# Optimization experiments

Hardware: AMD Instinct MI355X
Metric: run time of the kernel (lower is better)

The kernel has to match this reference:

```python
import jax, jax.numpy as jnp
import numpy as np

NUM_STEPS = 8
ADD_IDENTITY = True
EPS = 1e-12
STANDARDIZE = True


def setup_inputs() -> dict:
    key = jax.random.key(0)
    N = 4096
    E = 65536  # avg degree 16
    edge_index = jax.random.randint(key, (2, E), 0, N, dtype=jnp.int64 if jax.config.jax_enable_x64 else jnp.int32)
    edge_weight = jnp.ones((E,), dtype=jnp.float32)
    return {"edge_index": edge_index, "edge_weight": edge_weight, "num_nodes": N}


def reference(edge_index, edge_weight, num_nodes):
    # A[i,j] = sum of edge_weight over edges (row=i, col=j); scipy sums duplicates,
    # and segment_sum does the same.
    row, col = edge_index[0], edge_index[1]
    # deg_j = column sums of A (A.sum(axis=0))
    deg = jax.ops.segment_sum(edge_weight, col, num_segments=num_nodes)
    deg = jnp.maximum(deg, EPS)
    # M = A @ D^{-1}:  M[row, col] = w / deg[col]
    w = edge_weight / deg[col]  # [E]

    # Carry dense propagator P = M^t, extract diagonals for t = 1..NUM_STEPS.
    P0 = jnp.eye(num_nodes, dtype=jnp.float32)  # [N, N]

    def step(P, _):
        # P_new[i, :] = sum_{edges (i=row, j=col)} w_e * P[j, :]
        P = jax.ops.segment_sum(w[:, None] * P[col], row, num_segments=num_nodes)
        return P, jnp.diagonal(P)

    _, diags = jax.lax.scan(step, P0, None, length=NUM_STEPS)  # [T, N]

    X = diags.T  # [N, T]
    if ADD_IDENTITY:
        X = jnp.concatenate([jnp.ones((num_nodes, 1), dtype=jnp.float32), X], axis=1)
    if STANDARDIZE:
        mean = X.mean(axis=0, keepdims=True)
        std = jnp.maximum(X.std(axis=0, keepdims=True), 1e-6)  # ddof=0 == unbiased=False
        X = (X - mean) / std
    return X
```

## Files before the change

kernel.cpp:

```cpp
#include <hip/hip_runtime.h>

#define NN 4096
#define TSTEPS 8
#define EPSW 1e-12f
#define SLABW 512
#define NSLAB 8
#define LSLAB 9
#define SLAB_ELEMS ((size_t)NN * SLABW)

typedef unsigned int uint32;
typedef uint32 uint4v __attribute__((ext_vector_type(4)));

__device__ __forceinline__ uint32 bf16rn(float f) {
  uint32 b = __float_as_uint(f);
  return (b + 0x7FFFu + ((b >> 16) & 1u)) >> 16;
}
__device__ __forceinline__ float bf2f(ushort u) {
  return __uint_as_float(((uint32)u) << 16);
}
__device__ __forceinline__ float rdlanef(float v, int k) {
  return __uint_as_float(__builtin_amdgcn_readlane(__float_as_uint(v), k));
}
__device__ __forceinline__ int sphys(int c) {
  int blk = c >> 3;
  return ((blk ^ ((blk >> 3) & 7)) << 3) | (c & 7);
}

__global__ __launch_bounds__(256) void deg_counts_kernel(
    const int* __restrict__ rows, const int* __restrict__ cols,
    const float* __restrict__ ew, float* __restrict__ deg,
    int* __restrict__ counts, int E) {
  int e = blockIdx.x * 256 + threadIdx.x;
  if (e >= E) return;
  atomicAdd(deg + cols[e], ew[e]);
  atomicAdd(counts + rows[e], 1);
}

__global__ __launch_bounds__(1024) void scan_kernel(const int* __restrict__ counts,
                                                    int* __restrict__ row_ptr) {
  __shared__ int sm[1024];
  int tid = threadIdx.x;
  int b = tid * 4;
  int c0 = counts[b], c1 = counts[b + 1], c2 = counts[b + 2], c3 = counts[b + 3];
  sm[tid] = c0 + c1 + c2 + c3;
  __syncthreads();
  for (int off = 1; off < 1024; off <<= 1) {
    int v = (tid >= off) ? sm[tid - off] : 0;
    __syncthreads();
    sm[tid] += v;
    __syncthreads();
  }
  int excl = (tid == 0) ? 0 : sm[tid - 1];
  row_ptr[b]     = excl;
  row_ptr[b + 1] = excl + c0;
  row_ptr[b + 2] = excl + c0 + c1;
  row_ptr[b + 3] = excl + c0 + c1 + c2;
  if (tid == 1023) row_ptr[NN] = sm[1023];
}

__global__ __launch_bounds__(256) void csr_scatter_kernel(
    const int* __restrict__ rows, const int* __restrict__ cols,
    const float* __restrict__ ew, const float* __restrict__ deg,
    const int* __restrict__ row_ptr, int* __restrict__ fill,
    int* __restrict__ col_s, float* __restrict__ w_s,
    float* __restrict__ diags, int E) {
  int e = blockIdx.x * 256 + threadIdx.x;
  if (e >= E) return;
  int r = rows[e], c = cols[e];
  float w = ew[e] / fmaxf(deg[c], EPSW);
  int pos = row_ptr[r] + atomicAdd(fill + r, 1);
  col_s[pos] = c;
  w_s[pos] = w;
  if (r == c) atomicAdd(diags + r, w);
}

__global__ __launch_bounds__(64) void m2_csr_kernel(
    const int* __restrict__ row_ptr, const int* __restrict__ col_s,
    const float* __restrict__ w_s, ushort* __restrict__ dst,
    float* __restrict__ diags) {
  int i = blockIdx.x;
  int tid = threadIdx.x;
  __shared__ float acc[NN];
  float4 z4 = make_float4(0.f, 0.f, 0.f, 0.f);
#pragma unroll
  for (int k = 0; k < 16; ++k) *(float4*)(acc + k * 256 + tid * 4) = z4;
  int e0 = row_ptr[i], e1 = row_ptr[i + 1];
  __syncthreads();
  for (int base = e0; base < e1; base += 64) {
    int cnt = min(64, e1 - base);
    int myc = 0;
    float myw = 0.f;
    if (tid < cnt) { myc = col_s[base + tid]; myw = w_s[base + tid]; }
    for (int e = 0; e < cnt; ++e) {
      int j = __builtin_amdgcn_readlane(myc, e);
      float we = rdlanef(myw, e);
      int f0 = row_ptr[j], f1 = row_ptr[j + 1];
      for (int f = f0 + tid; f < f1; f += 64)
        atomicAdd(acc + sphys(col_s[f]), we * w_s[f]);
    }
  }
  __syncthreads();
  if (tid == 0) diags[NN + i] = acc[sphys(i)];
#pragma unroll
  for (int p = 0; p < 8; ++p) {
    int c = p * SLABW + tid * 8;
    int ph = sphys(c);
    float4 lo = *(const float4*)(acc + ph);
    float4 hi = *(const float4*)(acc + ph + 4);
    uint4v o;
    o.x = bf16rn(lo.x) | (bf16rn(lo.y) << 16);
    o.y = bf16rn(lo.z) | (bf16rn(lo.w) << 16);
    o.z = bf16rn(hi.x) | (bf16rn(hi.y) << 16);
    o.w = bf16rn(hi.z) | (bf16rn(hi.w) << 16);
    __builtin_nontemporal_store(
        o, (uint4v*)(dst + (size_t)p * SLAB_ELEMS + (size_t)i * SLABW + tid * 8));
  }
}

#define FMA8(u, w)                                            \
  do {                                                        \
    _Pragma("unroll") for (int q = 0; q < 4; ++q) {           \
      acc[2 * q]     += (w) * __uint_as_float((u)[q] << 16);  \
      acc[2 * q + 1] += (w) * __uint_as_float((u)[q] & 0xFFFF0000u); \
    }                                                         \
  } while (0)

__global__ __launch_bounds__(256) void spmm_kernel(
    const ushort* __restrict__ src, ushort* __restrict__ dst,
    const int* __restrict__ row_ptr, const int* __restrict__ col_s,
    const float* __restrict__ w_s, float* __restrict__ diags, int tIdx) {
  int b = blockIdx.x;
  int slab = b & (NSLAB - 1);
  int wv = threadIdx.x >> 6;
  int lane = threadIdx.x & 63;
  int i = ((b >> 3) << 2) | wv;
  int e0 = row_ptr[i], e1 = row_ptr[i + 1];
  __shared__ int sc_all[4][64];
  __shared__ float sw_all[4][64];
  int* sc = sc_all[wv];
  float* sw = sw_all[wv];
  float acc[8];
#pragma unroll
  for (int q = 0; q < 8; ++q) acc[q] = 0.f;
  const ushort* sbase = src + (size_t)slab * SLAB_ELEMS + lane * 8;

  for (int base = e0; base < e1; base += 64) {
    int cnt = min(64, e1 - base);
    if (lane < cnt) {
      sc[lane] = col_s[base + lane];
      sw[lane] = w_s[base + lane];
    }
    int k = 0;
    for (; k + 8 <= cnt; k += 8) {
      uint4v u0 = *(const uint4v*)(sbase + ((size_t)sc[k]     << LSLAB));
      uint4v u1 = *(const uint4v*)(sbase + ((size_t)sc[k + 1] << LSLAB));
      uint4v u2 = *(const uint4v*)(sbase + ((size_t)sc[k + 2] << LSLAB));
      uint4v u3 = *(const uint4v*)(sbase + ((size_t)sc[k + 3] << LSLAB));
      uint4v u4 = *(const uint4v*)(sbase + ((size_t)sc[k + 4] << LSLAB));
      uint4v u5 = *(const uint4v*)(sbase + ((size_t)sc[k + 5] << LSLAB));
      uint4v u6 = *(const uint4v*)(sbase + ((size_t)sc[k + 6] << LSLAB));
      uint4v u7 = *(const uint4v*)(sbase + ((size_t)sc[k + 7] << LSLAB));
      float w0 = sw[k], w1 = sw[k + 1], w2 = sw[k + 2], w3 = sw[k + 3];
      float w4 = sw[k + 4], w5 = sw[k + 5], w6 = sw[k + 6], w7 = sw[k + 7];
      FMA8(u0, w0); FMA8(u1, w1); FMA8(u2, w2); FMA8(u3, w3);
      FMA8(u4, w4); FMA8(u5, w5); FMA8(u6, w6); FMA8(u7, w7);
    }
    for (; k + 4 <= cnt; k += 4) {
      uint4v u0 = *(const uint4v*)(sbase + ((size_t)sc[k]     << LSLAB));
      uint4v u1 = *(const uint4v*)(sbase + ((size_t)sc[k + 1] << LSLAB));
      uint4v u2 = *(const uint4v*)(sbase + ((size_t)sc[k + 2] << LSLAB));
      uint4v u3 = *(const uint4v*)(sbase + ((size_t)sc[k + 3] << LSLAB));
      float w0 = sw[k], w1 = sw[k + 1], w2 = sw[k + 2], w3 = sw[k + 3];
      FMA8(u0, w0); FMA8(u1, w1); FMA8(u2, w2); FMA8(u3, w3);
    }
    for (; k < cnt; ++k) {
      uint4v u = *(const uint4v*)(sbase + ((size_t)sc[k] << LSLAB));
      float w = sw[k];
      FMA8(u, w);
    }
  }

  uint4v o;
#pragma unroll
  for (int q = 0; q < 4; ++q)
    o[q] = bf16rn(acc[2 * q]) | (bf16rn(acc[2 * q + 1]) << 16);
  __builtin_nontemporal_store(
      o, (uint4v*)(dst + (size_t)slab * SLAB_ELEMS + (size_t)i * SLABW + lane * 8));

  if ((i >> LSLAB) == slab) {
    int lc = i & (SLABW - 1);
    if ((lc >> 3) == lane) {
      int m = lc & 7;
      float v = acc[0];
      v = (m == 1) ? acc[1] : v;
      v = (m == 2) ? acc[2] : v;
      v = (m == 3) ? acc[3] : v;
      v = (m == 4) ? acc[4] : v;
      v = (m == 5) ? acc[5] : v;
      v = (m == 6) ? acc[6] : v;
      v = (m == 7) ? acc[7] : v;
      diags[tIdx * NN + i] = v;
    }
  }
}

__device__ __forceinline__ size_t slab_addr(int row, int col) {
  return ((size_t)(col >> LSLAB)) * SLAB_ELEMS + (size_t)row * SLABW + (col & (SLABW - 1));
}
__device__ __forceinline__ float elem8(uint4v lo, uint4v hi, int c) {
  uint32 u = (c < 8) ? lo[(c & 7) >> 1] : hi[(c & 7) >> 1];
  return __uint_as_float((c & 1) ? (u & 0xFFFF0000u) : (u << 16));
}

__global__ __launch_bounds__(256) void trace_kernel(
    const ushort* __restrict__ M2, const ushort* __restrict__ M3,
    const ushort* __restrict__ M4, float* __restrict__ diags) {
  int bid = blockIdx.x;
  int bi = bid >> 3, jc = bid & 7;
  int tid = threadIdx.x;
  __shared__ ushort b3[64 * 64], b4[64 * 64];
  __shared__ float red[4][4][64];
  int lr = tid >> 2, lc0 = (tid & 3) * 16;
  int r = tid & 63, jq = tid >> 6;
  float s5 = 0.f, s6 = 0.f, s7 = 0.f, s8 = 0.f;

  for (int it = 0; it < 8; ++it) {
    int bj = jc * 8 + it;
    {
      int gj = bj * 64 + lr;
      int gc = bi * 64 + lc0;
      size_t base = slab_addr(gj, gc);
      uint4v v3a = *(const uint4v*)(M3 + base);
      uint4v v3b = *(const uint4v*)(M3 + base + 8);
      uint4v v4a = *(const uint4v*)(M4 + base);
      uint4v v4b = *(const uint4v*)(M4 + base + 8);
      int cb0 = (lc0 >> 3) ^ (lr & 7);
      int cb1 = ((lc0 >> 3) + 1) ^ (lr & 7);
      *(uint4v*)(b3 + lr * 64 + cb0 * 8) = v3a;
      *(uint4v*)(b3 + lr * 64 + cb1 * 8) = v3b;
      *(uint4v*)(b4 + lr * 64 + cb0 * 8) = v4a;
      *(uint4v*)(b4 + lr * 64 + cb1 * 8) = v4b;
    }
    __syncthreads();
    int gi = bi * 64 + r;
    int gc0 = bj * 64 + jq * 16;
    size_t abase = slab_addr(gi, gc0);
    uint4v a2a = *(const uint4v*)(M2 + abase);
    uint4v a2b = *(const uint4v*)(M2 + abase + 8);
    uint4v a3a = *(const uint4v*)(M3 + abase);
    uint4v a3b = *(const uint4v*)(M3 + abase + 8);
    uint4v a4a = *(const uint4v*)(M4 + abase);
    uint4v a4b = *(const uint4v*)(M4 + abase + 8);
#pragma unroll
    for (int c = 0; c < 16; ++c) {
      int jj = jq * 16 + c;
      int idx = jj * 64 + ((((r >> 3) ^ (jj & 7)) << 3) | (r & 7));
      float bv3 = bf2f(b3[idx]);
      float bv4 = bf2f(b4[idx]);
      float av2 = elem8(a2a, a2b, c);
      float av3 = elem8(a3a, a3b, c);
      float av4 = elem8(a4a, a4b, c);
      s5 += av2 * bv3;
      s6 += av3 * bv3;
      s7 += av3 * bv4;
      s8 += av4 * bv4;
    }
    __syncthreads();
  }
  red[0][jq][r] = s5;
  red[1][jq][r] = s6;
  red[2][jq][r] = s7;
  red[3][jq][r] = s8;
  __syncthreads();
  if (tid < 64) {
    int gi = bi * 64 + tid;
#pragma unroll
    for (int v = 0; v < 4; ++v) {
      float s = red[v][0][tid] + red[v][1][tid] + red[v][2][tid] + red[v][3][tid];
      atomicAdd(diags + (4 + v) * NN + gi, s);
    }
  }
}

__global__ __launch_bounds__(256) void finalize_kernel(const float* __restrict__ diags,
                                                       float* __restrict__ out) {
  int k = blockIdx.x;
  int tid = threadIdx.x;
  float vals[16];
  float sum = 0.f, sq = 0.f;
#pragma unroll
  for (int j = 0; j < 16; ++j) {
    int i = j * 256 + tid;
    float v = (k == 0) ? 1.0f : diags[(k - 1) * NN + i];
    vals[j] = v;
    sum += v;
    sq += v * v;
  }
#pragma unroll
  for (int off = 32; off; off >>= 1) {
    sum += __shfl_down(sum, off);
    sq += __shfl_down(sq, off);
  }
  __shared__ float s0[4], s1[4];
  __shared__ float smean, sinv;
  int wid = tid >> 6, lane = tid & 63;
  if (lane == 0) { s0[wid] = sum; s1[wid] = sq; }
  __syncthreads();
  if (tid == 0) {
    float S = s0[0] + s0[1] + s0[2] + s0[3];
    float Q = s1[0] + s1[1] + s1[2] + s1[3];
    float mean = S / (float)NN;
    float var = Q / (float)NN - mean * mean;
    var = fmaxf(var, 0.f);
    float sd = fmaxf(sqrtf(var), 1e-6f);
    smean = mean;
    sinv = 1.f / sd;
  }
  __syncthreads();
#pragma unroll
  for (int j = 0; j < 16; ++j) {
    int i = j * 256 + tid;
    out[i * (TSTEPS + 1) + k] = (vals[j] - smean) * sinv;
  }
}

extern "C" void kernel_launch(void* const* d_in, const int* in_sizes, int n_in,
                              void* d_out, int out_size, void* d_ws, size_t ws_size,
                              hipStream_t stream) {
  const int* ei = (const int*)d_in[0];
  const float* ew = (const float*)d_in[1];
  int E = in_sizes[1];
  const int* rows = ei;
  const int* cols = ei + E;

  char* ws = (char*)d_ws;
  size_t off = 0;
  auto alloc = [&](size_t bytes) {
    void* p = ws + off;
    off = (off + bytes + 255) & ~(size_t)255;
    return p;
  };
  float* deg     = (float*)alloc(NN * 4);
  int*   counts  = (int*)alloc(NN * 4);
  int*   fill    = (int*)alloc(NN * 4);
  float* diags   = (float*)alloc((size_t)TSTEPS * NN * 4);
  size_t zbytes  = off;
  int*   row_ptr = (int*)alloc((NN + 1) * 4);
  int*   col_s   = (int*)alloc((size_t)E * 4);
  float* w_s     = (float*)alloc((size_t)E * 4);
  ushort* bufA   = (ushort*)alloc((size_t)NN * NN * 2);
  ushort* bufB   = (ushort*)alloc((size_t)NN * NN * 2);
  ushort* bufC   = (ushort*)alloc((size_t)NN * NN * 2);

  hipMemsetAsync(deg, 0, zbytes, stream);

  int eb = (E + 255) / 256;
  deg_counts_kernel<<<eb, 256, 0, stream>>>(rows, cols, ew, deg, counts, E);
  scan_kernel<<<1, 1024, 0, stream>>>(counts, row_ptr);
  csr_scatter_kernel<<<eb, 256, 0, stream>>>(rows, cols, ew, deg, row_ptr, fill,
                                             col_s, w_s, diags, E);

  m2_csr_kernel<<<NN, 64, 0, stream>>>(row_ptr, col_s, w_s, bufA, diags);
  spmm_kernel<<<(NN / 4) * NSLAB, 256, 0, stream>>>(bufA, bufB, row_ptr, col_s, w_s, diags, 2);
  spmm_kernel<<<(NN / 4) * NSLAB, 256, 0, stream>>>(bufB, bufC, row_ptr, col_s, w_s, diags, 3);
  trace_kernel<<<512, 256, 0, stream>>>(bufA, bufB, bufC, diags);

  finalize_kernel<<<TSTEPS + 1, 256, 0, stream>>>(diags, (float*)d_out);
}
```

Measured before the change: 148.3 us.

## Fuse CSR construction into one single-block kernel and use regular stores

Replaces the memset plus degree/count, scan, and scatter kernels with a single 1024-thread block that does degree, counts, scan, and scatter in shared memory with LDS atomics. It also zeroes the diagonal buffer itself. The intent is to remove launch overhead and global atomics, at the risk of serialising the edge work onto one CU. The nontemporal stores of bf16 propagator slabs become normal stores, so later kernels may hit them in cache.

```diff
diff --git a/kernel.cpp b/kernel.cpp
--- a/kernel.cpp
+++ b/kernel.cpp
@@ -26,22 +26,30 @@
   return ((blk ^ ((blk >> 3) & 7)) << 3) | (c & 7);
 }
 
-__global__ __launch_bounds__(256) void deg_counts_kernel(
+__global__ __launch_bounds__(1024) void build_kernel(
     const int* __restrict__ rows, const int* __restrict__ cols,
-    const float* __restrict__ ew, float* __restrict__ deg,
-    int* __restrict__ counts, int E) {
-  int e = blockIdx.x * 256 + threadIdx.x;
-  if (e >= E) return;
-  atomicAdd(deg + cols[e], ew[e]);
-  atomicAdd(counts + rows[e], 1);
-}
-
-__global__ __launch_bounds__(1024) void scan_kernel(const int* __restrict__ counts,
-                                                    int* __restrict__ row_ptr) {
+    const float* __restrict__ ew, int* __restrict__ row_ptr,
+    int* __restrict__ col_s, float* __restrict__ w_s,
+    float* __restrict__ diags, int E) {
+  __shared__ float degs[NN];
+  __shared__ int cnts[NN];
+  __shared__ int rp[NN];
   __shared__ int sm[1024];
   int tid = threadIdx.x;
+
+  for (int k = tid; k < NN; k += 1024) { degs[k] = 0.f; cnts[k] = 0; }
+  float4 z4 = make_float4(0.f, 0.f, 0.f, 0.f);
+  for (int k = tid; k < TSTEPS * NN / 4; k += 1024) ((float4*)diags)[k] = z4;
+  __syncthreads();
+
+  for (int e = tid; e < E; e += 1024) {
+    atomicAdd(&degs[cols[e]], ew[e]);
+    atomicAdd(&cnts[rows[e]], 1);
+  }
+  __syncthreads();
+
   int b = tid * 4;
-  int c0 = counts[b], c1 = counts[b + 1], c2 = counts[b + 2], c3 = counts[b + 3];
+  int c0 = cnts[b], c1 = cnts[b + 1], c2 = cnts[b + 2], c3 = cnts[b + 3];
   sm[tid] = c0 + c1 + c2 + c3;
   __syncthreads();
   for (int off = 1; off < 1024; off <<= 1) {
@@ -51,27 +59,26 @@
     __syncthreads();
   }
   int excl = (tid == 0) ? 0 : sm[tid - 1];
-  row_ptr[b]     = excl;
-  row_ptr[b + 1] = excl + c0;
-  row_ptr[b + 2] = excl + c0 + c1;
-  row_ptr[b + 3] = excl + c0 + c1 + c2;
-  if (tid == 1023) row_ptr[NN] = sm[1023];
-}
-
-__global__ __launch_bounds__(256) void csr_scatter_kernel(
-    const int* __restrict__ rows, const int* __restrict__ cols,
-    const float* __restrict__ ew, const float* __restrict__ deg,
-    const int* __restrict__ row_ptr, int* __restrict__ fill,
-    int* __restrict__ col_s, float* __restrict__ w_s,
-    float* __restrict__ diags, int E) {
-  int e = blockIdx.x * 256 + threadIdx.x;
-  if (e >= E) return;
-  int r = rows[e], c = cols[e];
-  float w = ew[e] / fmaxf(deg[c], EPSW);
-  int pos = row_ptr[r] + atomicAdd(fill + r, 1);
-  col_s[pos] = c;
-  w_s[pos] = w;
-  if (r == c) atomicAdd(diags + r, w);
+  rp[b] = excl;
+  rp[b + 1] = excl + c0;
+  rp[b + 2] = excl + c0 + c1;
+  rp[b + 3] = excl + c0 + c1 + c2;
+  row_ptr[b] = rp[b];
+  row_ptr[b + 1] = rp[b + 1];
+  row_ptr[b + 2] = rp[b + 2];
+  row_ptr[b + 3] = rp[b + 3];
+  cnts[b] = 0; cnts[b + 1] = 0; cnts[b + 2] = 0; cnts[b + 3] = 0;
+  if (tid == 1023) row_ptr[NN] = E;
+  __syncthreads();
+
+  for (int e = tid; e < E; e += 1024) {
+    int r = rows[e], c = cols[e];
+    float w = ew[e] / fmaxf(degs[c], EPSW);
+    int pos = rp[r] + atomicAdd(&cnts[r], 1);
+    col_s[pos] = c;
+    w_s[pos] = w;
+    if (r == c) atomicAdd(&diags[r], w);
+  }
 }
 
 __global__ __launch_bounds__(64) void m2_csr_kernel(
@@ -112,8 +119,7 @@
     o.y = bf16rn(lo.z) | (bf16rn(lo.w) << 16);
     o.z = bf16rn(hi.x) | (bf16rn(hi.y) << 16);
     o.w = bf16rn(hi.z) | (bf16rn(hi.w) << 16);
-    __builtin_nontemporal_store(
-        o, (uint4v*)(dst + (size_t)p * SLAB_ELEMS + (size_t)i * SLABW + tid * 8));
+    *(uint4v*)(dst + (size_t)p * SLAB_ELEMS + (size_t)i * SLABW + tid * 8) = o;
   }
 }
 
@@ -184,8 +190,7 @@
 #pragma unroll
   for (int q = 0; q < 4; ++q)
     o[q] = bf16rn(acc[2 * q]) | (bf16rn(acc[2 * q + 1]) << 16);
-  __builtin_nontemporal_store(
-      o, (uint4v*)(dst + (size_t)slab * SLAB_ELEMS + (size_t)i * SLABW + lane * 8));
+  *(uint4v*)(dst + (size_t)slab * SLAB_ELEMS + (size_t)i * SLABW + lane * 8) = o;
 
   if ((i >> LSLAB) == slab) {
     int lc = i & (SLABW - 1);
@@ -340,11 +345,7 @@
     off = (off + bytes + 255) & ~(size_t)255;
     return p;
   };
-  float* deg     = (float*)alloc(NN * 4);
-  int*   counts  = (int*)alloc(NN * 4);
-  int*   fill    = (int*)alloc(NN * 4);
   float* diags   = (float*)alloc((size_t)TSTEPS * NN * 4);
-  size_t zbytes  = off;
   int*   row_ptr = (int*)alloc((NN + 1) * 4);
   int*   col_s   = (int*)alloc((size_t)E * 4);
   float* w_s     = (float*)alloc((size_t)E * 4);
@@ -352,14 +353,8 @@
   ushort* bufB   = (ushort*)alloc((size_t)NN * NN * 2);
   ushort* bufC   = (ushort*)alloc((size_t)NN * NN * 2);
 
-  hipMemsetAsync(deg, 0, zbytes, stream);
-
-  int eb = (E + 255) / 256;
-  deg_counts_kernel<<<eb, 256, 0, stream>>>(rows, cols, ew, deg, counts, E);
-  scan_kernel<<<1, 1024, 0, stream>>>(counts, row_ptr);
-  csr_scatter_kernel<<<eb, 256, 0, stream>>>(rows, cols, ew, deg, row_ptr, fill,
-                                             col_s, w_s, diags, E);
-
+  build_kernel<<<1, 1024, 0, stream>>>(rows, cols, ew, row_ptr, col_s, w_s,
+                                       diags, E);
   m2_csr_kernel<<<NN, 64, 0, stream>>>(row_ptr, col_s, w_s, bufA, diags);
   spmm_kernel<<<(NN / 4) * NSLAB, 256, 0, stream>>>(bufA, bufB, row_ptr, col_s, w_s, diags, 2);
   spmm_kernel<<<(NN / 4) * NSLAB, 256, 0, stream>>>(bufB, bufC, row_ptr, col_s, w_s, diags, 3);
```

Result: slower. 295.8 us (+99.5%).
